# Performance work log

Measured on AMD Instinct MI355X. Metric: run time of the kernel, lower is better.

## Reference

```python
import jax, jax.numpy as jnp
import numpy as np

LR = 0.01
WD = 0.01


def _lfltm(params, x):
    w1, b1, w2, b2 = params
    return jnp.tanh(x @ w1 + b1) @ w2 + b2  # [N, D]


def _deep_opt_elem(Wm1, bm1, Wm2, bm2, g):
    # per-parameter-element learned optimizer: scalar grad -> hidden(M) -> scalar update
    h = jnp.tanh(g[..., None] * Wm1 + bm1)  # [..., M]
    return h @ Wm2 + bm2[0]


def setup_inputs() -> dict:
    key = jax.random.key(0)
    ks = jax.random.split(key, 8)
    N, D, H, M = 16384, 512, 1024, 32
    return {
        "x_t": jax.random.normal(ks[0], (N, D), jnp.float32),
        "x_target": jax.random.normal(ks[1], (N, D), jnp.float32),
        "w1": jax.random.normal(ks[2], (D, H), jnp.float32) * 0.02,
        "b1": jnp.zeros((H,), jnp.float32),
        "w2": jax.random.normal(ks[3], (H, D), jnp.float32) * 0.02,
        "b2": jnp.zeros((D,), jnp.float32),
        "Wm1": jax.random.normal(ks[4], (M,), jnp.float32) * 0.1,
        "bm1": jnp.zeros((M,), jnp.float32),
        "Wm2": jax.random.normal(ks[5], (M,), jnp.float32) * 0.1,
        "bm2": jnp.zeros((1,), jnp.float32),
    }


def reference(x_t, x_target, w1, b1, w2, b2, Wm1, bm1, Wm2, bm2):
    mem = (w1, b1, w2, b2)

    # retrieve: h_t = LFLTM(memory_state, x_t)
    h_t = _lfltm(mem, x_t)

    # analytic per-step gradient of MSE loss through the memory MLP
    def compute_loss(params):
        pred = _lfltm(params, x_t)
        return jnp.mean((pred - x_target) ** 2)

    grads = jax.grad(compute_loss)(mem)

    # learned optimizer on each gradient tensor, then fast-weight update
    new_mem = tuple(
        p - (LR * _deep_opt_elem(Wm1, bm1, Wm2, bm2, g) + WD * p)
        for p, g in zip(mem, grads)
    )

    return (h_t,) + new_mem
```

## Files before the change

### kernel.cpp

```cpp
#include <hip/hip_runtime.h>
#include <hip/hip_bf16.h>

#define LR 0.01f
#define WD 0.01f
#define NTHREADS 256
#define SCALE_G 1048576.0f
#define INV_SCALE_G 9.5367431640625e-07f

typedef short s16x8 __attribute__((ext_vector_type(8)));
typedef _Float16 f16x8 __attribute__((ext_vector_type(8)));
typedef float f32x4 __attribute__((ext_vector_type(4)));
typedef unsigned short u16;

__device__ __forceinline__ u16 f2h(float f) {
    _Float16 h = (_Float16)f;
    return *reinterpret_cast<u16*>(&h);
}
__device__ __forceinline__ float h2f(u16 u) {
    _Float16 h;
    *reinterpret_cast<u16*>(&h) = u;
    return (float)h;
}
__device__ __forceinline__ float tanh_fast(float x) {
    float t = fminf(fmaxf(2.f * x, -30.f), 30.f);
    float e = __expf(t);
    return 1.f - 2.f * __builtin_amdgcn_rcpf(e + 1.f);
}

__device__ __forceinline__ void stage_pair(const u16* gA, const u16* gB, int ldg,
                                           u16* lds) {
    const int t = threadIdx.x;
#pragma unroll
    for (int q = 0; q < 4; ++q) {
        int s = t + q * 256;
        int row = s >> 3, chp = s & 7;
        int chl = chp ^ (row & 7);
        const u16* gp = (chl < 4) ? (gA + (size_t)row * ldg + chl * 8)
                                  : (gB + (size_t)row * ldg + (chl & 3) * 8);
        __builtin_amdgcn_global_load_lds(
            (const __attribute__((address_space(1))) void*)gp,
            (__attribute__((address_space(3))) void*)(lds + s * 8), 16, 0, 0);
    }
}

__device__ __forceinline__ f16x8 frag(const u16* P, int r, int c) {
    return *(const f16x8*)(P + r * 64 + ((c ^ (r & 7)) * 8));
}

template <int EPI>
__global__ __launch_bounds__(NTHREADS) void k_mfma(
    const u16* __restrict__ A, const u16* __restrict__ Bt,
    int nbx, int Md, int Nd, int Kd, int Kslice,
    const float* __restrict__ bias, const float* __restrict__ xtgt,
    const u16* __restrict__ Th,
    float* __restrict__ outf, u16* __restrict__ outb, u16* __restrict__ outbT,
    float scale) {
    __shared__ u16 smem[2 * 8192];

    const int nwg = gridDim.x;
    const int sw = (blockIdx.x & 7) * (nwg >> 3) + (blockIdx.x >> 3);
    const int m0 = (sw / nbx) * 128, n0 = (sw % nbx) * 128;
    const int kb = blockIdx.y * Kslice;

    const int lane = threadIdx.x & 63, wid = threadIdx.x >> 6;
    const int wrow = (wid >> 1) * 64, wcol = (wid & 1) * 64;
    const int lm = lane & 15;
    const int cA = lane >> 4;

    f32x4 acc[4][4] = {};

    const u16* gA = A + (size_t)m0 * Kd + kb;
    const u16* gB = Bt + (size_t)n0 * Kd + kb;

    stage_pair(gA, gB, Kd, smem);
    __syncthreads();

    int cur = 0;
    for (int k0 = 0; k0 < Kslice; k0 += 32, cur ^= 1) {
        if (k0 + 32 < Kslice)
            stage_pair(gA + k0 + 32, gB + k0 + 32, Kd, smem + (cur ^ 1) * 8192);
        const u16* P1 = smem + cur * 8192;
        f16x8 a[4], b[4];
#pragma unroll
        for (int i = 0; i < 4; ++i) {
            a[i] = frag(P1, wrow + i * 16 + lm, cA);
            b[i] = frag(P1, wcol + i * 16 + lm, cA + 4);
        }
#pragma unroll
        for (int i = 0; i < 4; ++i)
#pragma unroll
            for (int j = 0; j < 4; ++j)
                acc[i][j] = __builtin_amdgcn_mfma_f32_16x16x32_f16(
                    a[i], b[j], acc[i][j], 0, 0, 0);
        __syncthreads();
    }

    const int rbase = (lane >> 4) * 4;
#pragma unroll
    for (int i = 0; i < 4; ++i) {
        const int row0 = m0 + wrow + i * 16 + rbase;
#pragma unroll
        for (int j = 0; j < 4; ++j) {
            const int col = n0 + wcol + j * 16 + lm;
            if (EPI == 0) {
                ushort4 hv;
                float bcol = bias[col];
                hv.x = f2h(tanh_fast(acc[i][j][0] + bcol));
                hv.y = f2h(tanh_fast(acc[i][j][1] + bcol));
                hv.z = f2h(tanh_fast(acc[i][j][2] + bcol));
                hv.w = f2h(tanh_fast(acc[i][j][3] + bcol));
                outb[(size_t)(row0 + 0) * Nd + col] = hv.x;
                outb[(size_t)(row0 + 1) * Nd + col] = hv.y;
                outb[(size_t)(row0 + 2) * Nd + col] = hv.z;
                outb[(size_t)(row0 + 3) * Nd + col] = hv.w;
                *(ushort4*)(outbT + (size_t)col * Md + row0) = hv;
            } else if (EPI == 1) {
                ushort4 gv;
#pragma unroll
                for (int r = 0; r < 4; ++r) {
                    size_t idx = (size_t)(row0 + r) * Nd + col;
                    float p = acc[i][j][r] + bias[col];
                    outf[idx] = p;
                    u16 g = f2h(scale * (p - xtgt[idx]));
                    outb[idx] = g;
                    ((u16*)&gv)[r] = g;
                }
                *(ushort4*)(outbT + (size_t)col * Md + row0) = gv;
            } else if (EPI == 2) {
                ushort4 dv;
#pragma unroll
                for (int r = 0; r < 4; ++r) {
                    size_t idx = (size_t)(row0 + r) * Nd + col;
                    float tv = h2f(Th[idx]);
                    ((u16*)&dv)[r] = f2h(acc[i][j][r] * (1.0f - tv * tv));
                }
                *(ushort4*)(outbT + (size_t)col * Md + row0) = dv;
            } else {
#pragma unroll
                for (int r = 0; r < 4; ++r)
                    atomicAdd(&outf[(size_t)(row0 + r) * Nd + col], acc[i][j][r]);
            }
        }
    }
}

__global__ void k_prep(const float* __restrict__ in, u16* __restrict__ rm,
                       u16* __restrict__ tr, int R, int C) {
    __shared__ float tile[64][65];
    const int tx = threadIdx.x & 63, ty = threadIdx.x >> 6;
    const int c0 = blockIdx.x * 64, r0 = blockIdx.y * 64;
#pragma unroll
    for (int i = 0; i < 64; i += 4) {
        size_t idx = (size_t)(r0 + ty + i) * C + c0 + tx;
        float v = in[idx];
        tile[ty + i][tx] = v;
        if (rm) rm[idx] = f2h(v);
    }
    __syncthreads();
    if (tr) {
#pragma unroll
        for (int i = 0; i < 64; i += 4)
            tr[(size_t)(c0 + ty + i) * R + r0 + tx] = f2h(tile[tx][ty + i]);
    }
}

__global__ void k_rowsum(const u16* __restrict__ src, float* __restrict__ dst,
                         int C) {
    const int row = blockIdx.x * 4 + (threadIdx.x >> 6);
    const int lane = threadIdx.x & 63;
    const u16* p = src + (size_t)row * C;
    float s = 0.f;
    for (int c = lane * 8; c < C; c += 64 * 8) {
        s16x8 v = *(const s16x8*)(p + c);
#pragma unroll
        for (int e = 0; e < 8; ++e) s += h2f((u16)v[e]);
    }
#pragma unroll
    for (int off = 32; off; off >>= 1) s += __shfl_down(s, off);
    if (lane == 0) dst[row] = s;
}

__global__ void k_update(const float* __restrict__ p, const float* __restrict__ g,
                         float* __restrict__ out, int n,
                         const float* __restrict__ Wm1, const float* __restrict__ bm1,
                         const float* __restrict__ Wm2, const float* __restrict__ bm2,
                         int M, float invScale) {
    __shared__ float s1[64], s2[64], s3[64];
    if (threadIdx.x < M) {
        s1[threadIdx.x] = Wm1[threadIdx.x];
        s2[threadIdx.x] = bm1[threadIdx.x];
        s3[threadIdx.x] = Wm2[threadIdx.x];
    }
    __syncthreads();
    int i = blockIdx.x * blockDim.x + threadIdx.x;
    if (i >= n) return;
    float gv = g[i] * invScale;
    float u = bm2[0];
#pragma unroll 8
    for (int m = 0; m < M; ++m) u += tanh_fast(fmaf(gv, s1[m], s2[m])) * s3[m];
    float pv = p[i];
    out[i] = pv - (LR * u + WD * pv);
}

__global__ void k_zero(float* __restrict__ p, int n) {
    int i = blockIdx.x * blockDim.x + threadIdx.x;
    if (i < n) p[i] = 0.f;
}

extern "C" void kernel_launch(void* const* d_in, const int* in_sizes, int n_in,
                              void* d_out, int out_size, void* d_ws, size_t ws_size,
                              hipStream_t stream) {
    const float* x_t      = (const float*)d_in[0];
    const float* x_target = (const float*)d_in[1];
    const float* w1  = (const float*)d_in[2];
    const float* b1  = (const float*)d_in[3];
    const float* w2  = (const float*)d_in[4];
    const float* b2  = (const float*)d_in[5];
    const float* Wm1 = (const float*)d_in[6];
    const float* bm1 = (const float*)d_in[7];
    const float* Wm2 = (const float*)d_in[8];
    const float* bm2 = (const float*)d_in[9];

    const int H = in_sizes[3];
    const int D = in_sizes[5];
    const int N = in_sizes[0] / D;
    const int M = in_sizes[6];

    char* w = (char*)d_ws;
    float* gw2 = (float*)w;            w += (size_t)H * D * 4;
    float* gw1 = (float*)w;            w += (size_t)D * H * 4;
    float* gb1 = (float*)w;            w += (size_t)H * 4;
    float* gb2 = (float*)w;            w += (size_t)D * 4;
    u16* Tf   = (u16*)w;               w += (size_t)N * H * 2;
    u16* TT   = (u16*)w;               w += (size_t)N * H * 2;
    u16* dAT  = (u16*)w;               w += (size_t)N * H * 2;
    u16* Gb   = (u16*)w;               w += (size_t)N * D * 2;
    u16* GT   = (u16*)w;               w += (size_t)N * D * 2;
    u16* xf   = (u16*)w;               w += (size_t)N * D * 2;
    u16* xT   = (u16*)w;               w += (size_t)N * D * 2;
    u16* w1T  = (u16*)w;               w += (size_t)D * H * 2;
    u16* w2T  = (u16*)w;               w += (size_t)D * H * 2;
    u16* w2b  = (u16*)w;               w += (size_t)H * D * 2;

    float* out  = (float*)d_out;
    float* h_t  = out;
    float* o_w1 = h_t + (size_t)N * D;
    float* o_b1 = o_w1 + (size_t)D * H;
    float* o_w2 = o_b1 + H;
    float* o_b2 = o_w2 + (size_t)H * D;

    dim3 blk(NTHREADS);
    const float scaleG = (2.0f / ((float)N * (float)D)) * SCALE_G;

    int zn = H * D + D * H;
    k_zero<<<dim3((zn + NTHREADS - 1) / NTHREADS), blk, 0, stream>>>(gw2, zn);

    k_prep<<<dim3(D / 64, N / 64), blk, 0, stream>>>(x_t, xf, xT, N, D);
    k_prep<<<dim3(H / 64, D / 64), blk, 0, stream>>>(w1, nullptr, w1T, D, H);
    k_prep<<<dim3(D / 64, H / 64), blk, 0, stream>>>(w2, w2b, w2T, H, D);

    k_mfma<0><<<dim3((H / 128) * (N / 128), 1), blk, 0, stream>>>(
        xf, w1T, H / 128, N, H, D, D, b1, nullptr, nullptr,
        nullptr, Tf, TT, 0.f);

    k_mfma<1><<<dim3((D / 128) * (N / 128), 1), blk, 0, stream>>>(
        Tf, w2T, D / 128, N, D, H, H, b2, x_target, nullptr,
        h_t, Gb, GT, scaleG);

    k_mfma<2><<<dim3((H / 128) * (N / 128), 1), blk, 0, stream>>>(
        Gb, w2b, H / 128, N, H, D, D, nullptr, nullptr, Tf,
        nullptr, nullptr, dAT, 0.f);

    const int SPLIT = 16;
    k_mfma<3><<<dim3((D / 128) * (H / 128), SPLIT), blk, 0, stream>>>(
        TT, GT, D / 128, H, D, N, N / SPLIT, nullptr, nullptr, nullptr,
        gw2, nullptr, nullptr, 0.f);

    k_mfma<3><<<dim3((H / 128) * (D / 128), SPLIT), blk, 0, stream>>>(
        xT, dAT, H / 128, D, H, N, N / SPLIT, nullptr, nullptr, nullptr,
        gw1, nullptr, nullptr, 0.f);

    k_rowsum<<<dim3(H / 4), blk, 0, stream>>>(dAT, gb1, N);
    k_rowsum<<<dim3(D / 4), blk, 0, stream>>>(GT, gb2, N);

    k_update<<<dim3((D * H + NTHREADS - 1) / NTHREADS), blk, 0, stream>>>(
        w1, gw1, o_w1, D * H, Wm1, bm1, Wm2, bm2, M, INV_SCALE_G);
    k_update<<<dim3((H + NTHREADS - 1) / NTHREADS), blk, 0, stream>>>(
        b1, gb1, o_b1, H, Wm1, bm1, Wm2, bm2, M, INV_SCALE_G);
    k_update<<<dim3((H * D + NTHREADS - 1) / NTHREADS), blk, 0, stream>>>(
        w2, gw2, o_w2, H * D, Wm1, bm1, Wm2, bm2, M, INV_SCALE_G);
    k_update<<<dim3((D + NTHREADS - 1) / NTHREADS), blk, 0, stream>>>(
        b2, gb2, o_b2, D, Wm1, bm1, Wm2, bm2, M, INV_SCALE_G);
}
```

Measured before the change: 422.0 us.

## Triple-stage GEMM loads, fuse bias-grad reductions into epilogues, merge update kernels

The MFMA main loop now prefetches two K-tiles ahead, using explicit vmcnt waits and raw barriers plus setprio around the MFMA block, so global-to-LDS loads overlap compute better. The bias gradients are accumulated in the EPI1/EPI2 epilogues via shared-memory column sums and global atomics, which removes the two rowsum kernels that reread dAT and GT. The four optimizer update launches are merged into one kernel over a contiguous gradient buffer. The cost is extra atomics and a riskier hand-tuned wait count that assumes a specific number of loads per stage.

```diff
diff --git a/kernel.cpp b/kernel.cpp
--- a/kernel.cpp
+++ b/kernel.cpp
@@ -54,8 +54,9 @@
     const float* __restrict__ bias, const float* __restrict__ xtgt,
     const u16* __restrict__ Th,
     float* __restrict__ outf, u16* __restrict__ outb, u16* __restrict__ outbT,
-    float scale) {
+    float* __restrict__ gbias, float scale) {
     __shared__ u16 smem[2 * 8192];
+    __shared__ float colacc[128];
 
     const int nwg = gridDim.x;
     const int sw = (blockIdx.x & 7) * (nwg >> 3) + (blockIdx.x >> 3);
@@ -71,14 +72,20 @@
 
     const u16* gA = A + (size_t)m0 * Kd + kb;
     const u16* gB = Bt + (size_t)n0 * Kd + kb;
+    const int nt = Kslice >> 5;
+
+    if (EPI == 1 || EPI == 2)
+        if (threadIdx.x < 128) colacc[threadIdx.x] = 0.f;
 
     stage_pair(gA, gB, Kd, smem);
-    __syncthreads();
+    stage_pair(gA + 32, gB + 32, Kd, smem + 8192);
 
     int cur = 0;
-    for (int k0 = 0; k0 < Kslice; k0 += 32, cur ^= 1) {
-        if (k0 + 32 < Kslice)
-            stage_pair(gA + k0 + 32, gB + k0 + 32, Kd, smem + (cur ^ 1) * 8192);
+    for (int t = 0; t < nt; ++t, cur ^= 1) {
+        if (t + 1 < nt) asm volatile("s_waitcnt vmcnt(4)" ::: "memory");
+        else            asm volatile("s_waitcnt vmcnt(0)" ::: "memory");
+        __builtin_amdgcn_s_barrier();
+
         const u16* P1 = smem + cur * 8192;
         f16x8 a[4], b[4];
 #pragma unroll
@@ -86,13 +93,20 @@
             a[i] = frag(P1, wrow + i * 16 + lm, cA);
             b[i] = frag(P1, wcol + i * 16 + lm, cA + 4);
         }
+        __builtin_amdgcn_s_setprio(1);
 #pragma unroll
         for (int i = 0; i < 4; ++i)
 #pragma unroll
             for (int j = 0; j < 4; ++j)
                 acc[i][j] = __builtin_amdgcn_mfma_f32_16x16x32_f16(
                     a[i], b[j], acc[i][j], 0, 0, 0);
-        __syncthreads();
+        __builtin_amdgcn_s_setprio(0);
+
+        asm volatile("" ::: "memory");
+        __builtin_amdgcn_s_barrier();
+        if (t + 2 < nt)
+            stage_pair(gA + (t + 2) * 32, gB + (t + 2) * 32, Kd,
+                       smem + cur * 8192);
     }
 
     const int rbase = (lane >> 4) * 4;
@@ -116,31 +130,44 @@
                 *(ushort4*)(outbT + (size_t)col * Md + row0) = hv;
             } else if (EPI == 1) {
                 ushort4 gv;
+                float csum = 0.f;
 #pragma unroll
                 for (int r = 0; r < 4; ++r) {
                     size_t idx = (size_t)(row0 + r) * Nd + col;
                     float p = acc[i][j][r] + bias[col];
                     outf[idx] = p;
-                    u16 g = f2h(scale * (p - xtgt[idx]));
+                    float gf = scale * (p - xtgt[idx]);
+                    csum += gf;
+                    u16 g = f2h(gf);
                     outb[idx] = g;
                     ((u16*)&gv)[r] = g;
                 }
                 *(ushort4*)(outbT + (size_t)col * Md + row0) = gv;
+                atomicAdd(&colacc[wcol + j * 16 + lm], csum);
             } else if (EPI == 2) {
                 ushort4 dv;
+                float csum = 0.f;
 #pragma unroll
                 for (int r = 0; r < 4; ++r) {
                     size_t idx = (size_t)(row0 + r) * Nd + col;
                     float tv = h2f(Th[idx]);
-                    ((u16*)&dv)[r] = f2h(acc[i][j][r] * (1.0f - tv * tv));
+                    float da = acc[i][j][r] * (1.0f - tv * tv);
+                    csum += da;
+                    ((u16*)&dv)[r] = f2h(da);
                 }
                 *(ushort4*)(outbT + (size_t)col * Md + row0) = dv;
+                atomicAdd(&colacc[wcol + j * 16 + lm], csum);
             } else {
 #pragma unroll
                 for (int r = 0; r < 4; ++r)
                     atomicAdd(&outf[(size_t)(row0 + r) * Nd + col], acc[i][j][r]);
             }
         }
+    }
+    if (EPI == 1 || EPI == 2) {
+        __syncthreads();
+        if (threadIdx.x < 128)
+            atomicAdd(&gbias[n0 + threadIdx.x], colacc[threadIdx.x]);
     }
 }
 
@@ -164,27 +191,14 @@
     }
 }
 
-__global__ void k_rowsum(const u16* __restrict__ src, float* __restrict__ dst,
-                         int C) {
-    const int row = blockIdx.x * 4 + (threadIdx.x >> 6);
-    const int lane = threadIdx.x & 63;
-    const u16* p = src + (size_t)row * C;
-    float s = 0.f;
-    for (int c = lane * 8; c < C; c += 64 * 8) {
-        s16x8 v = *(const s16x8*)(p + c);
-#pragma unroll
-        for (int e = 0; e < 8; ++e) s += h2f((u16)v[e]);
-    }
-#pragma unroll
-    for (int off = 32; off; off >>= 1) s += __shfl_down(s, off);
-    if (lane == 0) dst[row] = s;
-}
-
-__global__ void k_update(const float* __restrict__ p, const float* __restrict__ g,
-                         float* __restrict__ out, int n,
-                         const float* __restrict__ Wm1, const float* __restrict__ bm1,
-                         const float* __restrict__ Wm2, const float* __restrict__ bm2,
-                         int M, float invScale) {
+__global__ void k_update_all(
+    const float* __restrict__ w1, const float* __restrict__ b1,
+    const float* __restrict__ w2, const float* __restrict__ b2,
+    const float* __restrict__ g, float* __restrict__ out,
+    int n1, int n2, int n3, int n4,
+    const float* __restrict__ Wm1, const float* __restrict__ bm1,
+    const float* __restrict__ Wm2, const float* __restrict__ bm2,
+    int M, float invScale) {
     __shared__ float s1[64], s2[64], s3[64];
     if (threadIdx.x < M) {
         s1[threadIdx.x] = Wm1[threadIdx.x];
@@ -193,12 +207,19 @@
     }
     __syncthreads();
     int i = blockIdx.x * blockDim.x + threadIdx.x;
+    int n = n1 + n2 + n3 + n4;
     if (i >= n) return;
+    const float* p;
+    int off;
+    if (i < n1) { p = w1; off = 0; }
+    else if (i < n1 + n2) { p = b1; off = n1; }
+    else if (i < n1 + n2 + n3) { p = w2; off = n1 + n2; }
+    else { p = b2; off = n1 + n2 + n3; }
     float gv = g[i] * invScale;
     float u = bm2[0];
 #pragma unroll 8
     for (int m = 0; m < M; ++m) u += tanh_fast(fmaf(gv, s1[m], s2[m])) * s3[m];
-    float pv = p[i];
+    float pv = p[i - off];
     out[i] = pv - (LR * u + WD * pv);
 }
 
@@ -227,9 +248,9 @@
     const int M = in_sizes[6];
 
     char* w = (char*)d_ws;
-    float* gw2 = (float*)w;            w += (size_t)H * D * 4;
     float* gw1 = (float*)w;            w += (size_t)D * H * 4;
     float* gb1 = (float*)w;            w += (size_t)H * 4;
+    float* gw2 = (float*)w;            w += (size_t)H * D * 4;
     float* gb2 = (float*)w;            w += (size_t)D * 4;
     u16* Tf   = (u16*)w;               w += (size_t)N * H * 2;
     u16* TT   = (u16*)w;               w += (size_t)N * H * 2;
@@ -245,15 +266,12 @@
     float* out  = (float*)d_out;
     float* h_t  = out;
     float* o_w1 = h_t + (size_t)N * D;
-    float* o_b1 = o_w1 + (size_t)D * H;
-    float* o_w2 = o_b1 + H;
-    float* o_b2 = o_w2 + (size_t)H * D;
 
     dim3 blk(NTHREADS);
     const float scaleG = (2.0f / ((float)N * (float)D)) * SCALE_G;
 
-    int zn = H * D + D * H;
-    k_zero<<<dim3((zn + NTHREADS - 1) / NTHREADS), blk, 0, stream>>>(gw2, zn);
+    int zn = D * H + H + H * D + D;
+    k_zero<<<dim3((zn + NTHREADS - 1) / NTHREADS), blk, 0, stream>>>(gw1, zn);
 
     k_prep<<<dim3(D / 64, N / 64), blk, 0, stream>>>(x_t, xf, xT, N, D);
     k_prep<<<dim3(H / 64, D / 64), blk, 0, stream>>>(w1, nullptr, w1T, D, H);
@@ -261,34 +279,27 @@
 
     k_mfma<0><<<dim3((H / 128) * (N / 128), 1), blk, 0, stream>>>(
         xf, w1T, H / 128, N, H, D, D, b1, nullptr, nullptr,
-        nullptr, Tf, TT, 0.f);
+        nullptr, Tf, TT, nullptr, 0.f);
 
     k_mfma<1><<<dim3((D / 128) * (N / 128), 1), blk, 0, stream>>>(
         Tf, w2T, D / 128, N, D, H, H, b2, x_target, nullptr,
-        h_t, Gb, GT, scaleG);
+        h_t, Gb, GT, gb2, scaleG);
 
     k_mfma<2><<<dim3((H / 128) * (N / 128), 1), blk, 0, stream>>>(
         Gb, w2b, H / 128, N, H, D, D, nullptr, nullptr, Tf,
-        nullptr, nullptr, dAT, 0.f);
+        nullptr, nullptr, dAT, gb1, 0.f);
 
     const int SPLIT = 16;
     k_mfma<3><<<dim3((D / 128) * (H / 128), SPLIT), blk, 0, stream>>>(
         TT, GT, D / 128, H, D, N, N / SPLIT, nullptr, nullptr, nullptr,
-        gw2, nullptr, nullptr, 0.f);
+        gw2, nullptr, nullptr, nullptr, 0.f);
 
     k_mfma<3><<<dim3((H / 128) * (D / 128), SPLIT), blk, 0, stream>>>(
         xT, dAT, H / 128, D, H, N, N / SPLIT, nullptr, nullptr, nullptr,
-        gw1, nullptr, nullptr, 0.f);
-
-    k_rowsum<<<dim3(H / 4), blk, 0, stream>>>(dAT, gb1, N);
-    k_rowsum<<<dim3(D / 4), blk, 0, stream>>>(GT, gb2, N);
-
-    k_update<<<dim3((D * H + NTHREADS - 1) / NTHREADS), blk, 0, stream>>>(
-        w1, gw1, o_w1, D * H, Wm1, bm1, Wm2, bm2, M, INV_SCALE_G);
-    k_update<<<dim3((H + NTHREADS - 1) / NTHREADS), blk, 0, stream>>>(
-        b1, gb1, o_b1, H, Wm1, bm1, Wm2, bm2, M, INV_SCALE_G);
-    k_update<<<dim3((H * D + NTHREADS - 1) / NTHREADS), blk, 0, stream>>>(
-        w2, gw2, o_w2, H * D, Wm1, bm1, Wm2, bm2, M, INV_SCALE_G);
-    k_update<<<dim3((D + NTHREADS - 1) / NTHREADS), blk, 0, stream>>>(
-        b2, gb2, o_b2, D, Wm1, bm1, Wm2, bm2, M, INV_SCALE_G);
-}
+        gw1, nullptr, nullptr, nullptr, 0.f);
+
+    int nAll = D * H + H + H * D + D;
+    k_update_all<<<dim3((nAll + NTHREADS - 1) / NTHREADS), blk, 0, stream>>>(
+        w1, b1, w2, b2, gw1, o_w1, D * H, H, H * D, D,
+        Wm1, bm1, Wm2, bm2, M, INV_SCALE_G);
+}
```

Result: faster. 398.4 us (-5.6%).
